# Kernel tuning notes

Measured on AMD Instinct MI355X. Metric: run time of the kernel, lower is better.

Reference implementation:

```python
import jax, jax.numpy as jnp
import numpy as np

NTOK, NINP, NREL = 50257, 512, 200
N, L, EPS = 1024, 64, 32  # n sequences, seq length, edges per sequence
E = N * EPS               # m.sum()


def setup_inputs() -> dict:
    key = jax.random.key(0)
    k1, k2, k3, k4 = jax.random.split(key, 4)
    seq = jax.random.randint(k1, (N, L), 0, NTOK, dtype=jnp.int32)
    m = jnp.full((N,), EPS, dtype=jnp.int32)          # edges per sequence (constant -> static E)
    rel = jax.random.randint(k2, (E,), 0, NREL, dtype=jnp.int32)
    emb = jax.random.normal(k3, (NTOK, NINP), dtype=jnp.float32)          # nn.Embedding weight
    W = 0.01 * jax.random.normal(k4, (NREL, NINP), dtype=jnp.float32)     # nn.Linear weight
    b = jnp.zeros((NREL,), dtype=jnp.float32)                             # nn.Linear bias
    return {"seq": seq, "m": m, "rel": rel, "emb": emb, "W": W, "b": b}


def reference(seq, m, rel, emb, W, b):
    # logit = linear(embedding(seq).sum(1))
    h = emb[seq].sum(axis=1)                    # (N, NINP) gather + segment-sum over tokens
    logit = h @ W.T + b                         # (N, NREL)

    # multi-label mask: mask[i, r] = True iff some edge of sequence i has relation r
    n_seq = m.shape[0]
    idx = jnp.repeat(jnp.arange(n_seq), m, total_repeat_length=rel.shape[0])  # (E,)
    mask = jnp.zeros((n_seq, logit.shape[1]), dtype=bool).at[idx, rel].set(True)

    # sum of logsigmoid on positive labels + log(1+1e-5 - sigmoid) on negatives, / len(seq)
    logp = jnp.sum(jnp.where(mask,
                             jax.nn.log_sigmoid(logit),
                             jnp.log(1.0 + 1e-5 - jax.nn.sigmoid(logit)))) / seq.shape[0]
    acc = jnp.mean(((logit > 0.5) == mask).astype(jnp.float32))
    return logp, acc
```

## Files before the change

kernel.cpp:

```cpp
#include <hip/hip_runtime.h>

#define NINP 512
#define NREL 200
#define LSEQ 64
#define WT_LD 256
#define SPB 4

__global__ __launch_bounds__(256) void gather_prep_kernel(
    const int* __restrict__ seq,
    const float* __restrict__ emb,
    const float* __restrict__ W,
    float4* __restrict__ part,
    float* __restrict__ Wt,
    int N, int L)
{
    const int b = blockIdx.x;
    const int t = threadIdx.x;

    if (b < NINP / 2) {
        #pragma unroll
        for (int j = 0; j < 2; ++j) {
            const int k = b * 2 + j;
            Wt[k * WT_LD + t] = (t < NREL) ? W[t * NINP + k] : 0.f;
        }
        return;
    }

    __shared__ int    toks[32];
    __shared__ float4 hpart[2][NINP / 4];

    const int gb = b - NINP / 2;
    const int s  = gb >> 1;
    const int hs = gb & 1;
    const int grp = t >> 7;
    const int e   = t & 127;

    if (t < 32) toks[t] = seq[s * LSEQ + hs * 32 + t];
    __syncthreads();

    float4 acc = make_float4(0.f, 0.f, 0.f, 0.f);
    #pragma unroll
    for (int batch = 0; batch < 2; ++batch) {
        const int base = grp * 16 + batch * 8;
        float4 v[8];
        #pragma unroll
        for (int j = 0; j < 8; ++j) {
            const int tok = __builtin_amdgcn_readfirstlane(toks[base + j]);
            v[j] = ((const float4*)(emb + (long)tok * NINP))[e];
        }
        float4 s01, s23, s45, s67;
        s01.x = v[0].x + v[1].x; s01.y = v[0].y + v[1].y; s01.z = v[0].z + v[1].z; s01.w = v[0].w + v[1].w;
        s23.x = v[2].x + v[3].x; s23.y = v[2].y + v[3].y; s23.z = v[2].z + v[3].z; s23.w = v[2].w + v[3].w;
        s45.x = v[4].x + v[5].x; s45.y = v[4].y + v[5].y; s45.z = v[4].z + v[5].z; s45.w = v[4].w + v[5].w;
        s67.x = v[6].x + v[7].x; s67.y = v[6].y + v[7].y; s67.z = v[6].z + v[7].z; s67.w = v[6].w + v[7].w;
        acc.x += (s01.x + s23.x) + (s45.x + s67.x);
        acc.y += (s01.y + s23.y) + (s45.y + s67.y);
        acc.z += (s01.z + s23.z) + (s45.z + s67.z);
        acc.w += (s01.w + s23.w) + (s45.w + s67.w);
    }
    hpart[grp][e] = acc;
    __syncthreads();

    if (t < 128) {
        float4 lo = hpart[0][t];
        float4 hi = hpart[1][t];
        lo.x += hi.x; lo.y += hi.y; lo.z += hi.z; lo.w += hi.w;
        part[(long)gb * 128 + t] = lo;
    }
}

__global__ __launch_bounds__(1024) void loss_kernel(
    const float4* __restrict__ part,
    const float* __restrict__ Wt,
    const int* __restrict__ rel,
    const float* __restrict__ bias,
    float* __restrict__ out,
    int N, int eps)
{
    __shared__ float h_lds[SPB][NINP];
    __shared__ unsigned int maskbits[SPB][8];
    __shared__ float pd[SPB][4][256];
    __shared__ float red_logp[16];
    __shared__ float red_acc[16];

    const int i0 = blockIdx.x * SPB;
    const int t  = threadIdx.x;

    if (t < 512) {
        const int s = t >> 7, e = t & 127;
        float4 lo = part[(long)(i0 + s) * 256 + e];
        float4 hi = part[(long)(i0 + s) * 256 + 128 + e];
        float4 c;
        c.x = lo.x + hi.x; c.y = lo.y + hi.y; c.z = lo.z + hi.z; c.w = lo.w + hi.w;
        ((float4*)h_lds)[t] = c;
    }
    if (t >= 512 && t < 512 + SPB * 8) ((unsigned int*)maskbits)[t - 512] = 0u;
    __syncthreads();
    if (t < SPB * 32) {
        const int s = t >> 5, j = t & 31;
        if (j < eps) {
            int r = rel[(i0 + s) * eps + j];
            atomicOr(&maskbits[s][r >> 5], 1u << (r & 31));
        }
    }

    const int kslice = t >> 8;
    const int r      = t & 255;
    float d0 = 0.f, d1 = 0.f, d2 = 0.f, d3 = 0.f;
    const float4* h40 = (const float4*)h_lds[0];
    const float4* h41 = (const float4*)h_lds[1];
    const float4* h42 = (const float4*)h_lds[2];
    const float4* h43 = (const float4*)h_lds[3];
    #pragma unroll 4
    for (int k4 = kslice * 32; k4 < kslice * 32 + 32; ++k4) {
        const int k = k4 * 4;
        const float w0 = Wt[(k + 0) * WT_LD + r];
        const float w1 = Wt[(k + 1) * WT_LD + r];
        const float w2 = Wt[(k + 2) * WT_LD + r];
        const float w3 = Wt[(k + 3) * WT_LD + r];
        const float4 hv0 = h40[k4];
        const float4 hv1 = h41[k4];
        const float4 hv2 = h42[k4];
        const float4 hv3 = h43[k4];
        d0 += w0 * hv0.x + w1 * hv0.y + w2 * hv0.z + w3 * hv0.w;
        d1 += w0 * hv1.x + w1 * hv1.y + w2 * hv1.z + w3 * hv1.w;
        d2 += w0 * hv2.x + w1 * hv2.y + w2 * hv2.z + w3 * hv2.w;
        d3 += w0 * hv3.x + w1 * hv3.y + w2 * hv3.z + w3 * hv3.w;
    }
    pd[0][kslice][r] = d0;
    pd[1][kslice][r] = d1;
    pd[2][kslice][r] = d2;
    pd[3][kslice][r] = d3;
    __syncthreads();

    float term = 0.f, match = 0.f;
    if (t < NREL) {
        const float bt = bias[t];
        #pragma unroll
        for (int s = 0; s < SPB; ++s) {
            const float dot = ((pd[s][0][t] + pd[s][1][t]) +
                               (pd[s][2][t] + pd[s][3][t])) + bt;
            const unsigned mb = (maskbits[s][t >> 5] >> (t & 31)) & 1u;
            float tr;
            if (mb) {
                tr = fminf(dot, 0.f) - log1pf(expf(-fabsf(dot)));
            } else {
                tr = logf(1e-5f + 1.f / (1.f + expf(dot)));
            }
            term  += tr;
            match += (((dot > 0.5f) ? 1u : 0u) == mb) ? 1.f : 0.f;
        }
    }

    #pragma unroll
    for (int off = 32; off > 0; off >>= 1) {
        term  += __shfl_down(term,  off);
        match += __shfl_down(match, off);
    }
    const int wave = t >> 6;
    const int lane = t & 63;
    if (lane == 0) { red_logp[wave] = term; red_acc[wave] = match; }
    __syncthreads();
    if (t == 0) {
        float s = 0.f, a = 0.f;
        #pragma unroll
        for (int w = 0; w < 16; ++w) { s += red_logp[w]; a += red_acc[w]; }
        atomicAdd(out + 0, s / (float)N);
        atomicAdd(out + 1, a / ((float)N * (float)NREL));
    }
}

extern "C" void kernel_launch(void* const* d_in, const int* in_sizes, int n_in,
                              void* d_out, int out_size, void* d_ws, size_t ws_size,
                              hipStream_t stream) {
    const int*   seq = (const int*)d_in[0];
    const int*   m   = (const int*)d_in[1]; (void)m;
    const int*   rel = (const int*)d_in[2];
    const float* emb = (const float*)d_in[3];
    const float* W   = (const float*)d_in[4];
    const float* b   = (const float*)d_in[5];
    float* out = (float*)d_out;

    const int N   = in_sizes[1];
    const int L   = in_sizes[0] / N;
    const int eps = in_sizes[2] / N;

    float4* part = (float4*)d_ws;
    float*  Wt   = (float*)((char*)d_ws + (size_t)4 * 1024 * 1024);

    hipMemsetAsync(out, 0, 2 * sizeof(float), stream);
    gather_prep_kernel<<<NINP / 2 + N * 2, 256, 0, stream>>>(seq, emb, W, part, Wt, N, L);
    loss_kernel<<<N / SPB, 1024, 0, stream>>>(part, Wt, rel, b, out, N, eps);
}
```

Baseline: 181.9 us.

## Fuse embedding gather into loss kernel, split W transpose into its own kernel

The embedding gather-sum now runs inside the loss kernel: each 1024-thread block gathers the tokens for 2 sequences, reduces them in LDS, and goes straight to the GEMV and loss. This drops the intermediate partial-sum buffer and its global round trip. The W transpose moves to a separate small kernel. Fewer sequences per block (2 instead of 4) doubles the number of blocks but halves reuse of each Wt load, so Wt global reads double.

```diff
diff --git a/kernel.cpp b/kernel.cpp
--- a/kernel.cpp
+++ b/kernel.cpp
@@ -4,44 +4,51 @@
 #define NREL 200
 #define LSEQ 64
 #define WT_LD 256
-#define SPB 4
+#define SPB 2
 
-__global__ __launch_bounds__(256) void gather_prep_kernel(
-    const int* __restrict__ seq,
-    const float* __restrict__ emb,
+__global__ __launch_bounds__(256) void wt_kernel(
     const float* __restrict__ W,
-    float4* __restrict__ part,
-    float* __restrict__ Wt,
-    int N, int L)
+    float* __restrict__ Wt)
 {
     const int b = blockIdx.x;
     const int t = threadIdx.x;
+    #pragma unroll
+    for (int j = 0; j < 2; ++j) {
+        const int k = b * 2 + j;
+        Wt[k * WT_LD + t] = (t < NREL) ? W[t * NINP + k] : 0.f;
+    }
+}
 
-    if (b < NINP / 2) {
-        #pragma unroll
-        for (int j = 0; j < 2; ++j) {
-            const int k = b * 2 + j;
-            Wt[k * WT_LD + t] = (t < NREL) ? W[t * NINP + k] : 0.f;
-        }
-        return;
-    }
+__global__ __launch_bounds__(1024) void fused_kernel(
+    const int* __restrict__ seq,
+    const float* __restrict__ emb,
+    const float* __restrict__ Wt,
+    const int* __restrict__ rel,
+    const float* __restrict__ bias,
+    float* __restrict__ out,
+    int N, int eps)
+{
+    __shared__ int    toks[SPB * LSEQ];
+    __shared__ float4 hpart[8][128];
+    __shared__ float  h_lds[SPB][NINP];
+    __shared__ unsigned int maskbits[SPB][8];
+    __shared__ float  pd[SPB][4][256];
+    __shared__ float  red_logp[16];
+    __shared__ float  red_acc[16];
 
-    __shared__ int    toks[32];
-    __shared__ float4 hpart[2][NINP / 4];
+    const int i0 = blockIdx.x * SPB;
+    const int t  = threadIdx.x;
 
-    const int gb = b - NINP / 2;
-    const int s  = gb >> 1;
-    const int hs = gb & 1;
-    const int grp = t >> 7;
-    const int e   = t & 127;
-
-    if (t < 32) toks[t] = seq[s * LSEQ + hs * 32 + t];
+    if (t < SPB * LSEQ) toks[t] = seq[i0 * LSEQ + t];
+    if (t >= 512 && t < 512 + SPB * 8) ((unsigned int*)maskbits)[t - 512] = 0u;
     __syncthreads();
 
+    const int g = t >> 7;
+    const int e = t & 127;
     float4 acc = make_float4(0.f, 0.f, 0.f, 0.f);
     #pragma unroll
     for (int batch = 0; batch < 2; ++batch) {
-        const int base = grp * 16 + batch * 8;
+        const int base = g * 16 + batch * 8;
         float4 v[8];
         #pragma unroll
         for (int j = 0; j < 8; ++j) {
@@ -58,59 +65,36 @@
         acc.z += (s01.z + s23.z) + (s45.z + s67.z);
         acc.w += (s01.w + s23.w) + (s45.w + s67.w);
     }
-    hpart[grp][e] = acc;
+    hpart[g][e] = acc;
     __syncthreads();
 
-    if (t < 128) {
-        float4 lo = hpart[0][t];
-        float4 hi = hpart[1][t];
-        lo.x += hi.x; lo.y += hi.y; lo.z += hi.z; lo.w += hi.w;
-        part[(long)gb * 128 + t] = lo;
-    }
-}
-
-__global__ __launch_bounds__(1024) void loss_kernel(
-    const float4* __restrict__ part,
-    const float* __restrict__ Wt,
-    const int* __restrict__ rel,
-    const float* __restrict__ bias,
-    float* __restrict__ out,
-    int N, int eps)
-{
-    __shared__ float h_lds[SPB][NINP];
-    __shared__ unsigned int maskbits[SPB][8];
-    __shared__ float pd[SPB][4][256];
-    __shared__ float red_logp[16];
-    __shared__ float red_acc[16];
-
-    const int i0 = blockIdx.x * SPB;
-    const int t  = threadIdx.x;
-
-    if (t < 512) {
-        const int s = t >> 7, e = t & 127;
-        float4 lo = part[(long)(i0 + s) * 256 + e];
-        float4 hi = part[(long)(i0 + s) * 256 + 128 + e];
+    if (t < SPB * 128) {
+        const int s = t >> 7, ee = t & 127;
+        float4 a0 = hpart[4 * s + 0][ee];
+        float4 a1 = hpart[4 * s + 1][ee];
+        float4 a2 = hpart[4 * s + 2][ee];
+        float4 a3 = hpart[4 * s + 3][ee];
         float4 c;
-        c.x = lo.x + hi.x; c.y = lo.y + hi.y; c.z = lo.z + hi.z; c.w = lo.w + hi.w;
+        c.x = (a0.x + a1.x) + (a2.x + a3.x);
+        c.y = (a0.y + a1.y) + (a2.y + a3.y);
+        c.z = (a0.z + a1.z) + (a2.z + a3.z);
+        c.w = (a0.w + a1.w) + (a2.w + a3.w);
         ((float4*)h_lds)[t] = c;
     }
-    if (t >= 512 && t < 512 + SPB * 8) ((unsigned int*)maskbits)[t - 512] = 0u;
-    __syncthreads();
-    if (t < SPB * 32) {
-        const int s = t >> 5, j = t & 31;
+    if (t >= 512 && t < 512 + SPB * 32) {
+        const int s = (t - 512) >> 5, j = (t - 512) & 31;
         if (j < eps) {
             int r = rel[(i0 + s) * eps + j];
             atomicOr(&maskbits[s][r >> 5], 1u << (r & 31));
         }
     }
+    __syncthreads();
 
     const int kslice = t >> 8;
     const int r      = t & 255;
-    float d0 = 0.f, d1 = 0.f, d2 = 0.f, d3 = 0.f;
+    float d0 = 0.f, d1 = 0.f;
     const float4* h40 = (const float4*)h_lds[0];
     const float4* h41 = (const float4*)h_lds[1];
-    const float4* h42 = (const float4*)h_lds[2];
-    const float4* h43 = (const float4*)h_lds[3];
     #pragma unroll 4
     for (int k4 = kslice * 32; k4 < kslice * 32 + 32; ++k4) {
         const int k = k4 * 4;
@@ -120,17 +104,11 @@
         const float w3 = Wt[(k + 3) * WT_LD + r];
         const float4 hv0 = h40[k4];
         const float4 hv1 = h41[k4];
-        const float4 hv2 = h42[k4];
-        const float4 hv3 = h43[k4];
         d0 += w0 * hv0.x + w1 * hv0.y + w2 * hv0.z + w3 * hv0.w;
         d1 += w0 * hv1.x + w1 * hv1.y + w2 * hv1.z + w3 * hv1.w;
-        d2 += w0 * hv2.x + w1 * hv2.y + w2 * hv2.z + w3 * hv2.w;
-        d3 += w0 * hv3.x + w1 * hv3.y + w2 * hv3.z + w3 * hv3.w;
     }
     pd[0][kslice][r] = d0;
     pd[1][kslice][r] = d1;
-    pd[2][kslice][r] = d2;
-    pd[3][kslice][r] = d3;
     __syncthreads();
 
     float term = 0.f, match = 0.f;
@@ -182,13 +160,11 @@
     float* out = (float*)d_out;
 
     const int N   = in_sizes[1];
-    const int L   = in_sizes[0] / N;
     const int eps = in_sizes[2] / N;
 
-    float4* part = (float4*)d_ws;
-    float*  Wt   = (float*)((char*)d_ws + (size_t)4 * 1024 * 1024);
+    float* Wt = (float*)d_ws;
 
     hipMemsetAsync(out, 0, 2 * sizeof(float), stream);
-    gather_prep_kernel<<<NINP / 2 + N * 2, 256, 0, stream>>>(seq, emb, W, part, Wt, N, L);
-    loss_kernel<<<N / SPB, 1024, 0, stream>>>(part, Wt, rel, b, out, N, eps);
+    wt_kernel<<<NINP / 2, 256, 0, stream>>>(W, Wt);
+    fused_kernel<<<N / SPB, 1024, 0, stream>>>(seq, emb, Wt, rel, b, out, N, eps);
 }
```

Result: no change. 181.9 us (+0.0%).
